# Optimization experiments

Hardware: AMD Instinct MI355X
Metric: run time of the kernel (lower is better)

Reference implementation:

```python
import jax, jax.numpy as jnp
import numpy as np

N_NODES = 2048
N_EDGES = 32768
DIM = 256
HEADS = 4

PARAM_SHAPES = {
    'Wq': (DIM, DIM), 'bq': (DIM,), 'Wk': (DIM, DIM), 'bk': (DIM,),
    'Wv': (DIM, DIM), 'bv': (DIM,), 'Wo': (DIM, DIM), 'bo': (DIM,),
    'gd_W1': (4, 3), 'gd_b1': (3,), 'gd_W2': (3, HEADS), 'gd_b2': (HEADS,),
    'tw_W1': (2 * DIM, DIM), 'tw_b1': (DIM,), 'tw_W2': (DIM, DIM), 'tw_b2': (DIM,),
    'ne_W1': (4 * DIM, 2 * DIM), 'ne_b1': (2 * DIM,), 'ne_W2': (2 * DIM, DIM), 'ne_b2': (DIM,),
    'att_W1': (2 * DIM // HEADS, 2 * DIM // HEADS), 'att_b1': (2 * DIM // HEADS,),
    'att_W2': (DIM // HEADS, 2 * DIM // HEADS), 'att_b2': (DIM // HEADS,),
    'pe_W': (DIM, DIM), 'pe_b': (DIM,), 'pq_W': (DIM, DIM), 'pq_b': (DIM,),
    'pv_W': (DIM, DIM), 'pv_b': (DIM,),
    'pr_W1': (2 * DIM, 2 * DIM), 'pr_b1': (2 * DIM,), 'pr_W2': (2 * DIM, DIM), 'pr_b2': (DIM,),
}


def _lin(x, W, b):
    return x @ W + b


def _mlp2(x, W1, b1, W2, b2):  # Linear-ReLU-Linear (build_mlp, on_last=False)
    return _lin(jnp.maximum(_lin(x, W1, b1), 0.0), W2, b2)


def setup_inputs() -> dict:
    key = jax.random.key(0)
    ks = iter(jax.random.split(key, 64))
    rng = np.random.default_rng(0)
    half = N_EDGES // 2
    s = rng.integers(0, N_NODES, half)
    d = rng.integers(0, N_NODES, half)
    # reciprocal edge pairs so the reverse-edge lookup path is exercised
    edge_index = jnp.asarray(np.stack([np.concatenate([s, d]), np.concatenate([d, s])]), dtype=jnp.int32)
    inp = {
        'node_f': jax.random.normal(next(ks), (N_NODES, DIM), jnp.float32),
        'edge_f': jax.random.normal(next(ks), (N_EDGES, DIM), jnp.float32),
        'coords': jax.random.normal(next(ks), (N_NODES, 3), jnp.float32),
        'edge_index': edge_index,
        'num_heads': HEADS,
    }
    for name, shp in PARAM_SHAPES.items():
        inp[name] = jax.random.normal(next(ks), shp, jnp.float32) * 0.02
    return inp


def _forward(node_f, edge_f, coords, edge_index, num_heads,
             Wq, bq, Wk, bk, Wv, bv, Wo, bo,
             gd_W1, gd_b1, gd_W2, gd_b2,
             tw_W1, tw_b1, tw_W2, tw_b2,
             ne_W1, ne_b1, ne_W2, ne_b2,
             att_W1, att_b1, att_W2, att_b2,
             pe_W, pe_b, pq_W, pq_b, pv_W, pv_b,
             pr_W1, pr_b1, pr_W2, pr_b2):
    N, Dn = node_f.shape
    E, De = edge_f.shape
    H = num_heads
    dh = Wq.shape[1] // H
    src, dst = edge_index[0], edge_index[1]

    # --- NodeUpdate: distance-aware MHSA over all node pairs (batch=1) ---
    q = _lin(node_f, Wq, bq).reshape(N, H, dh)
    k = _lin(node_f, Wk, bk).reshape(N, H, dh)
    v = _lin(node_f, Wv, bv).reshape(N, H, dh)
    diff = coords[:, None, :] - coords[None, :, :]  # [N,N,3]
    sq = jnp.sum(diff * diff, axis=-1, keepdims=True)
    dist = jnp.where(sq > 0, jnp.sqrt(jnp.where(sq > 0, sq, 1.0)), 0.0)
    dmask = _mlp2(jnp.concatenate([diff, dist], -1), gd_W1, gd_b1, gd_W2, gd_b2)  # [N,N,H]
    scores = jnp.einsum('nhd,mhd->hnm', q, k) / float(dh) ** 0.5 + dmask.transpose(2, 0, 1)
    attn = jax.nn.softmax(scores, axis=-1)
    mhsa = _lin(jnp.einsum('hnm,mhd->nhd', attn, v).reshape(N, H * dh), Wo, bo)

    # --- TwinningEdgeAttention: per-node mean of outgoing / incoming edge feats ---
    ones = jnp.ones((E,), edge_f.dtype)
    cnt_s = jnp.maximum(jax.ops.segment_sum(ones, src, num_segments=N), 1.0)
    cnt_d = jnp.maximum(jax.ops.segment_sum(ones, dst, num_segments=N), 1.0)
    sub_mean = jax.ops.segment_sum(edge_f, src, num_segments=N) / cnt_s[:, None]
    obj_mean = jax.ops.segment_sum(edge_f, dst, num_segments=N) / cnt_d[:, None]
    edge_att = jax.nn.sigmoid(_mlp2(jnp.concatenate([sub_mean, obj_mean], -1), tw_W1, tw_b1, tw_W2, tw_b2))
    node_out = jnp.maximum(mhsa, 0.0) * edge_att  # [N, Dn]

    # --- GraphEdgeAttenNetwork ---
    x_i = node_f[src]
    x_j = node_f[dst]
    # reverse-edge matching (vectorized replacement of the python double loop)
    table = jnp.zeros((N * N,), jnp.int32).at[src * N + dst].set(jnp.arange(E, dtype=jnp.int32) + 1)
    rev = table[dst * N + src]
    rev_feat = jnp.where((rev > 0)[:, None], edge_f[jnp.maximum(rev - 1, 0)], 0.0)
    edge_out = _mlp2(jnp.concatenate([x_i, edge_f, rev_feat, x_j], -1), ne_W1, ne_b1, ne_W2, ne_b2)

    value = _lin(x_j, pv_W, pv_b)  # [E, Da]
    query = _lin(x_i, pq_W, pq_b).reshape(E, Dn // H, H)
    edgep = _lin(edge_f, pe_W, pe_b).reshape(E, De // H, H)
    qe = jnp.concatenate([query, edgep], axis=1)  # [E, d_n+d_e, H]
    # conv1d(kernel=1) MLP over channel axis, ReLU between layers
    h = jnp.maximum(jnp.einsum('ech,oc->eoh', qe, att_W1) + att_b1[None, :, None], 0.0)
    prob = jax.nn.softmax(jnp.einsum('ech,oc->eoh', h, att_W2) + att_b2[None, :, None], axis=1)  # [E, d_o, H]
    msg = prob.reshape(E, -1) * value
    agg = jax.ops.segment_max(msg, src, num_segments=N)
    agg = jnp.where(jnp.isfinite(agg), agg, 0.0)  # empty segments -> 0 (torch scatter_max fill)
    xx = _mlp2(jnp.concatenate([node_f, agg], -1), pr_W1, pr_b1, pr_W2, pr_b2)
    return node_out, edge_out, xx


def reference(node_f, edge_f, coords, edge_index, num_heads,
              Wq, bq, Wk, bk, Wv, bv, Wo, bo,
              gd_W1, gd_b1, gd_W2, gd_b2,
              tw_W1, tw_b1, tw_W2, tw_b2,
              ne_W1, ne_b1, ne_W2, ne_b2,
              att_W1, att_b1, att_W2, att_b2,
              pe_W, pe_b, pq_W, pq_b, pv_W, pv_b,
              pr_W1, pr_b1, pr_W2, pr_b2):
    return _forward(node_f, edge_f, coords, edge_index, num_heads,
                    Wq, bq, Wk, bk, Wv, bv, Wo, bo,
                    gd_W1, gd_b1, gd_W2, gd_b2,
                    tw_W1, tw_b1, tw_W2, tw_b2,
                    ne_W1, ne_b1, ne_W2, ne_b2,
                    att_W1, att_b1, att_W2, att_b2,
                    pe_W, pe_b, pq_W, pq_b, pv_W, pv_b,
                    pr_W1, pr_b1, pr_W2, pr_b2)
```

## Files before the change

kernel.cpp:

```cpp
#include <hip/hip_runtime.h>

#define NN 2048
#define NE 32768
#define DIM 256
#define NH 4

typedef unsigned short u16;
typedef __attribute__((ext_vector_type(4))) unsigned short u16x4;
typedef __attribute__((ext_vector_type(8))) short bf16x8;
typedef __attribute__((ext_vector_type(4))) float f32x4;

typedef __attribute__((address_space(1))) const unsigned int g_as1;
typedef __attribute__((address_space(3))) unsigned int l_as3;

__device__ __forceinline__ void gload16(const u16* g, u16* l) {
  __builtin_amdgcn_global_load_lds((g_as1*)g, (l_as3*)l, 16, 0, 0);
}

__device__ __forceinline__ u16 f2bf(float f) {
  unsigned u = __float_as_uint(f);
  unsigned r = u + 0x7FFFu + ((u >> 16) & 1u);
  return (u16)(r >> 16);
}
__device__ __forceinline__ float bf2f(u16 b) {
  return __uint_as_float(((unsigned)b) << 16);
}

struct GB { const u16* A; const int* idx; long ld; long aoffz; };

template<int BNF, int EPI>
__global__ __launch_bounds__(256) void gemm_bf(
    GB ga, const u16* __restrict__ Bt, long bld, long boffz,
    const float* __restrict__ bias, void* __restrict__ Cp, long ldc, long coffz,
    int K, float scale)
{
  __shared__ u16 As[128 * 64];
  __shared__ u16 Bs[32 * BNF * 64];

  const int tid = threadIdx.x;
  const int wid = tid >> 6, lane = tid & 63;
  const int bz = blockIdx.z;
  const int m0 = blockIdx.y * 128;
  const int n0 = blockIdx.x * (32 * BNF);
  const int wr = wid >> 1, wc = wid & 1;
  const int l15 = lane & 15, l4 = lane >> 4;

  const u16* asrc[4];
  #pragma unroll
  for (int c = 0; c < 4; ++c) {
    int rl = c*32 + wid*8 + (lane >> 3);
    int row = ga.idx ? ga.idx[m0 + rl] : (m0 + rl);
    int c16s = (lane & 7) ^ (rl & 7);
    asrc[c] = ga.A + ga.aoffz * bz + (long)row * ga.ld + c16s * 8;
  }
  const u16* bsrc[BNF];
  #pragma unroll
  for (int c = 0; c < BNF; ++c) {
    int rl = c*32 + wid*8 + (lane >> 3);
    int c16s = (lane & 7) ^ (rl & 7);
    bsrc[c] = Bt + boffz * bz + (long)(n0 + rl) * bld + c16s * 8;
  }

  f32x4 acc[4][BNF] = {};

  for (int k0 = 0; k0 < K; k0 += 64) {
    #pragma unroll
    for (int c = 0; c < 4; ++c)
      gload16(asrc[c] + k0, &As[(c*32 + wid*8) * 64]);
    #pragma unroll
    for (int c = 0; c < BNF; ++c)
      gload16(bsrc[c] + k0, &Bs[(c*32 + wid*8) * 64]);
    __syncthreads();

    #pragma unroll
    for (int kk = 0; kk < 2; ++kk) {
      bf16x8 af[4], bfr[BNF];
      #pragma unroll
      for (int i = 0; i < 4; ++i) {
        int r = wr*64 + i*16 + l15;
        af[i] = *(const bf16x8*)&As[r*64 + (((kk*4 + l4) ^ (r & 7)) * 8)];
      }
      #pragma unroll
      for (int j = 0; j < BNF; ++j) {
        int r = wc*(16*BNF) + j*16 + l15;
        bfr[j] = *(const bf16x8*)&Bs[r*64 + (((kk*4 + l4) ^ (r & 7)) * 8)];
      }
      #pragma unroll
      for (int i = 0; i < 4; ++i)
        #pragma unroll
        for (int j = 0; j < BNF; ++j)
          acc[i][j] = __builtin_amdgcn_mfma_f32_16x16x32_bf16(af[i], bfr[j], acc[i][j], 0, 0, 0);
    }
    __syncthreads();
  }

  #pragma unroll
  for (int j = 0; j < BNF; ++j) {
    const int col = n0 + wc*(16*BNF) + j*16 + l15;
    const float bb = bias ? bias[col] : 0.f;
    #pragma unroll
    for (int i = 0; i < 4; ++i) {
      #pragma unroll
      for (int r = 0; r < 4; ++r) {
        const int m = m0 + wr*64 + i*16 + l4*4 + r;
        float v = acc[i][j][r] * scale + bb;
        if constexpr (EPI == 1) v = fmaxf(v, 0.f);
        if constexpr (EPI == 2) v = 1.f / (1.f + expf(-v));
        if constexpr (EPI == 0 || EPI == 2)
          ((float*)Cp)[coffz*bz + (long)m*ldc + col] = v;
        else if constexpr (EPI == 4)
          ((u16*)Cp)[((long)(col & 3) * NE + m) * ldc + (col >> 2) + coffz] = f2bf(v);
        else if constexpr (EPI == 8) {
          if (col < 256)
            ((float*)Cp)[(long)m*256 + (col & 3)*64 + (col >> 2)] = v;
          else {
            u16* qb = (u16*)((float*)Cp + (long)NN*256);
            int c2 = col - 256;
            qb[((long)(c2 & 3)*NN + m)*64 + (c2 >> 2)] = f2bf(v);
          }
        }
        else
          ((u16*)Cp)[coffz*bz + (long)m*ldc + col] = f2bf(v);
      }
    }
  }
}

__global__ __launch_bounds__(256) void flash_k(
    const u16* __restrict__ qkv,
    const u16* __restrict__ vT,
    const float4* __restrict__ pk,
    const float* __restrict__ gW1, const float* __restrict__ gb1,
    const float* __restrict__ gW2, const float* __restrict__ gb2,
    float* __restrict__ Op,
    float2* __restrict__ ml)
{
  __shared__ u16 Qls[64*64];
  __shared__ u16 Kls[128*64];
  __shared__ u16 Vls[2][64*64];
  __shared__ u16 Pls[4][16*128];

  const int tid = threadIdx.x, wid = tid >> 6, lane = tid & 63;
  const int h  = blockIdx.x & 3;
  const int m0 = (blockIdx.x >> 2) * 64;
  const int part = blockIdx.y;
  const int l15 = lane & 15, l4 = lane >> 4;
  const int rl8 = wid*8 + (lane >> 3);
  const int c8  = lane & 7;

  #pragma unroll
  for (int c = 0; c < 2; ++c) {
    int r = c*32 + rl8;
    gload16(qkv + (long)(m0 + r)*768 + h*64 + ((c8 ^ (r & 7))*8), &Qls[(c*32 + wid*8)*64]);
  }
  __syncthreads();
  bf16x8 qf[2];
  {
    int r = wid*16 + l15;
    qf[0] = *(const bf16x8*)&Qls[r*64 + (((0*4 + l4) ^ (r & 7))*8)];
    qf[1] = *(const bf16x8*)&Qls[r*64 + (((1*4 + l4) ^ (r & 7))*8)];
  }

  const float b10 = gb1[0], b11 = gb1[1], b12 = gb1[2];
  const float w30 = gW1[9], w31 = gW1[10], w32 = gW1[11];
  const float w20 = gW2[0*4+h], w21 = gW2[1*4+h], w22 = gW2[2*4+h];
  const float b2h = gb2[h];
  float4 rp0[4], rp1[4];
  #pragma unroll
  for (int r = 0; r < 4; ++r) {
    int qrow = m0 + wid*16 + l4*4 + r;
    rp0[r] = pk[qrow*2]; rp1[r] = pk[qrow*2 + 1];
  }

  float mrun[4] = {-1e30f, -1e30f, -1e30f, -1e30f};
  float lrun[4] = {};
  f32x4 pa[4] = {};

  for (int t = 0; t < 2; ++t) {
    const int n0 = part*256 + t*128;
    #pragma unroll
    for (int c = 0; c < 4; ++c) {
      int r = c*32 + rl8;
      gload16(qkv + (long)(n0 + r)*768 + 256 + h*64 + ((c8 ^ (r & 7))*8),
              &Kls[(c*32 + wid*8)*64]);
    }
    #pragma unroll
    for (int hh = 0; hh < 2; ++hh)
      #pragma unroll
      for (int c = 0; c < 2; ++c) {
        int r = c*32 + rl8;
        gload16(vT + (long)(h*64 + r)*NN + n0 + hh*64 + ((c8 ^ (r & 7))*8),
                &Vls[hh][(c*32 + wid*8)*64]);
      }
    __syncthreads();

    f32x4 sa[8] = {};
    #pragma unroll
    for (int kk = 0; kk < 2; ++kk) {
      #pragma unroll
      for (int j = 0; j < 8; ++j) {
        int r = j*16 + l15;
        bf16x8 bf = *(const bf16x8*)&Kls[r*64 + (((kk*4 + l4) ^ (r & 7))*8)];
        sa[j] = __builtin_amdgcn_mfma_f32_16x16x32_bf16(qf[kk], bf, sa[j], 0, 0, 0);
      }
    }

    float rowmx[4] = {-1e30f, -1e30f, -1e30f, -1e30f};
    #pragma unroll
    for (int j = 0; j < 8; ++j) {
      int n = n0 + j*16 + l15;
      float4 cp0 = pk[n*2], cp1 = pk[n*2 + 1];
      #pragma unroll
      for (int r = 0; r < 4; ++r) {
        float dot = rp0[r].x*cp0.x + rp0[r].y*cp0.y + rp0[r].z*cp0.z;
        float sq = rp0[r].w + cp0.w - 2.f*dot;
        float dist = sq > 0.f ? sq * __frsqrt_rn(sq) : 0.f;
        float h0 = fmaxf(b10 + rp1[r].x - cp1.x + dist*w30, 0.f);
        float h1 = fmaxf(b11 + rp1[r].y - cp1.y + dist*w31, 0.f);
        float h2 = fmaxf(b12 + rp1[r].z - cp1.z + dist*w32, 0.f);
        float s = sa[j][r]*0.125f + b2h + h0*w20 + h1*w21 + h2*w22;
        sa[j][r] = s;
        rowmx[r] = fmaxf(rowmx[r], s);
      }
    }
    #pragma unroll
    for (int w = 1; w < 16; w <<= 1)
      #pragma unroll
      for (int r = 0; r < 4; ++r)
        rowmx[r] = fmaxf(rowmx[r], __shfl_xor(rowmx[r], w));

    float fac[4], rs[4] = {};
    #pragma unroll
    for (int r = 0; r < 4; ++r) {
      float mnew = fmaxf(mrun[r], rowmx[r]);
      fac[r] = __expf(mrun[r] - mnew);
      mrun[r] = mnew;
    }
    #pragma unroll
    for (int j = 0; j < 8; ++j)
      #pragma unroll
      for (int r = 0; r < 4; ++r) {
        float p = __expf(sa[j][r] - mrun[r]);
        sa[j][r] = p;
        rs[r] += p;
      }
    #pragma unroll
    for (int w = 1; w < 16; w <<= 1)
      #pragma unroll
      for (int r = 0; r < 4; ++r)
        rs[r] += __shfl_xor(rs[r], w);
    #pragma unroll
    for (int r = 0; r < 4; ++r) lrun[r] = lrun[r]*fac[r] + rs[r];
    #pragma unroll
    for (int j2 = 0; j2 < 4; ++j2)
      #pragma unroll
      for (int r = 0; r < 4; ++r)
        pa[j2][r] *= fac[r];

    #pragma unroll
    for (int j = 0; j < 8; ++j)
      #pragma unroll
      for (int r = 0; r < 4; ++r) {
        int qr = l4*4 + r, n = j*16 + l15;
        Pls[wid][qr*128 + (((n >> 3) ^ (qr & 7))*8) + (n & 7)] = f2bf(sa[j][r]);
      }
    #pragma unroll
    for (int ks = 0; ks < 4; ++ks) {
      bf16x8 paf = *(const bf16x8*)&Pls[wid][l15*128 + (((ks*4 + l4) ^ (l15 & 7))*8)];
      #pragma unroll
      for (int j2 = 0; j2 < 4; ++j2) {
        int r = j2*16 + l15;
        bf16x8 vf = *(const bf16x8*)&Vls[ks >> 1][r*64 + ((((ks & 1)*4 + l4) ^ (r & 7))*8)];
        pa[j2] = __builtin_amdgcn_mfma_f32_16x16x32_bf16(paf, vf, pa[j2], 0, 0, 0);
      }
    }
    __syncthreads();
  }

  #pragma unroll
  for (int j2 = 0; j2 < 4; ++j2)
    #pragma unroll
    for (int r = 0; r < 4; ++r) {
      int m = m0 + wid*16 + l4*4 + r;
      Op[((long)part*NN + m)*256 + h*64 + j2*16 + l15] = pa[j2][r];
    }
  if (l15 == 0) {
    #pragma unroll
    for (int r = 0; r < 4; ++r) {
      int m = m0 + wid*16 + l4*4 + r;
      ml[((long)part*NN + m)*4 + h] = make_float2(mrun[r], lrun[r]);
    }
  }
}

__global__ __launch_bounds__(256) void comb_k(const float* __restrict__ Op,
    const float2* __restrict__ ml, u16* __restrict__ attn) {
  int n = blockIdx.x, t = threadIdx.x, h = t >> 6;
  float m[8], l[8];
  #pragma unroll
  for (int p = 0; p < 8; ++p) { float2 v = ml[((long)p*NN + n)*4 + h]; m[p] = v.x; l[p] = v.y; }
  float M = m[0];
  #pragma unroll
  for (int p = 1; p < 8; ++p) M = fmaxf(M, m[p]);
  float L = 0.f, o = 0.f;
  #pragma unroll
  for (int p = 0; p < 8; ++p) {
    float w = __expf(m[p] - M);
    L += w * l[p];
    o += w * Op[((long)p*NN + n)*256 + t];
  }
  attn[(long)n*256 + t] = f2bf(o / L);
}

__global__ __launch_bounds__(64) void attedge_k(
    const u16* __restrict__ qN, const u16* __restrict__ ep,
    const float* __restrict__ valNp, const int* __restrict__ ei,
    const u16* __restrict__ W1, const float* __restrict__ b1,
    const u16* __restrict__ W2, const float* __restrict__ b2,
    u16* __restrict__ msgP)
{
  __shared__ u16 As[32*128];
  const int lane = threadIdx.x;
  const int h = blockIdx.y;
  const int e0 = blockIdx.x * 32;
  const int l15 = lane & 15, l4 = lane >> 4;

  #pragma unroll
  for (int p = 0; p < 8; ++p) {
    int R0 = p*4;
    int r  = R0 + (lane >> 4);
    int cd = lane & 15;
    int cs = ((cd & 7) ^ (r & 7)) | (cd & 8);
    const u16* src = (cs < 8)
        ? qN + ((long)h*NN + ei[e0 + r])*64 + cs*8
        : ep + ((long)h*NE + e0 + r)*64 + (cs & 7)*8;
    gload16(src, &As[R0*128]);
  }
  __syncthreads();

  f32x4 acc1[2][8] = {};
  #pragma unroll
  for (int kk = 0; kk < 4; ++kk) {
    bf16x8 af[2], bfr[8];
    #pragma unroll
    for (int i = 0; i < 2; ++i) {
      int rA = i*16 + l15;
      int cg = kk*4 + l4;
      int cd = ((cg & 7) ^ (rA & 7)) | (cg & 8);
      af[i] = *(const bf16x8*)&As[rA*128 + cd*8];
    }
    #pragma unroll
    for (int j = 0; j < 8; ++j)
      bfr[j] = *(const bf16x8*)&W1[(long)(j*16 + l15)*128 + kk*32 + l4*8];
    #pragma unroll
    for (int i = 0; i < 2; ++i)
      #pragma unroll
      for (int j = 0; j < 8; ++j)
        acc1[i][j] = __builtin_amdgcn_mfma_f32_16x16x32_bf16(af[i], bfr[j], acc1[i][j], 0, 0, 0);
  }
  __syncthreads();
  #pragma unroll
  for (int i = 0; i < 2; ++i)
    #pragma unroll
    for (int j = 0; j < 8; ++j) {
      int n = j*16 + l15;
      float bb = b1[n];
      #pragma unroll
      for (int r = 0; r < 4; ++r) {
        int m = i*16 + l4*4 + r;
        int cg = n >> 3;
        int cd = ((cg & 7) ^ (m & 7)) | (cg & 8);
        As[m*128 + cd*8 + (n & 7)] = f2bf(fmaxf(acc1[i][j][r] + bb, 0.f));
      }
    }
  __syncthreads();

  f32x4 acc2[2][4] = {};
  #pragma unroll
  for (int kk = 0; kk < 4; ++kk) {
    bf16x8 af[2], bfr[4];
    #pragma unroll
    for (int i = 0; i < 2; ++i) {
      int rA = i*16 + l15;
      int cg = kk*4 + l4;
      int cd = ((cg & 7) ^ (rA & 7)) | (cg & 8);
      af[i] = *(const bf16x8*)&As[rA*128 + cd*8];
    }
    #pragma unroll
    for (int j = 0; j < 4; ++j)
      bfr[j] = *(const bf16x8*)&W2[(long)(j*16 + l15)*128 + kk*32 + l4*8];
    #pragma unroll
    for (int i = 0; i < 2; ++i)
      #pragma unroll
      for (int j = 0; j < 4; ++j)
        acc2[i][j] = __builtin_amdgcn_mfma_f32_16x16x32_bf16(af[i], bfr[j], acc2[i][j], 0, 0, 0);
  }

  #pragma unroll
  for (int i = 0; i < 2; ++i) {
    float mx[4] = {-1e30f,-1e30f,-1e30f,-1e30f};
    #pragma unroll
    for (int j = 0; j < 4; ++j) {
      float bb = b2[j*16 + l15];
      #pragma unroll
      for (int r = 0; r < 4; ++r) {
        acc2[i][j][r] += bb;
        mx[r] = fmaxf(mx[r], acc2[i][j][r]);
      }
    }
    #pragma unroll
    for (int w = 1; w < 16; w <<= 1)
      #pragma unroll
      for (int r = 0; r < 4; ++r) mx[r] = fmaxf(mx[r], __shfl_xor(mx[r], w));
    float sum[4] = {};
    #pragma unroll
    for (int j = 0; j < 4; ++j)
      #pragma unroll
      for (int r = 0; r < 4; ++r) {
        float p = __expf(acc2[i][j][r] - mx[r]);
        acc2[i][j][r] = p; sum[r] += p;
      }
    #pragma unroll
    for (int w = 1; w < 16; w <<= 1)
      #pragma unroll
      for (int r = 0; r < 4; ++r) sum[r] += __shfl_xor(sum[r], w);
    #pragma unroll
    for (int r = 0; r < 4; ++r) {
      int m = i*16 + l4*4 + r;
      int e = e0 + m;
      int dst = ei[NE + e];
      float inv = 1.f / sum[r];
      #pragma unroll
      for (int j = 0; j < 4; ++j) {
        int o = j*16 + l15;
        float v = valNp[(long)dst*256 + h*64 + o];
        msgP[(long)e*256 + h*64 + o] = f2bf(acc2[i][j][r] * inv * v);
      }
    }
  }
}

__global__ __launch_bounds__(256) void gemm_ne(
    const u16* __restrict__ nbf, const u16* __restrict__ ebf, const u16* __restrict__ zbuf,
    const int* __restrict__ ei, const int* __restrict__ rev,
    const u16* __restrict__ Bt, const float* __restrict__ bias, u16* __restrict__ C)
{
  __shared__ u16 As[2][128 * 64];
  __shared__ u16 Bs[2][128 * 64];
  const int tid = threadIdx.x, wid = tid >> 6, lane = tid & 63;
  const int lin = blockIdx.y * 4 + blockIdx.x;
  const int xcd = lin & 7, seq = lin >> 3;
  const int m0 = (xcd*32 + (seq >> 2)) * 128;
  const int n0 = (seq & 3) * 128;
  const int wr = wid >> 1, wc = wid & 1, l15 = lane & 15, l4 = lane >> 4;

  const u16* asrc[4][4];
  #pragma unroll
  for (int c = 0; c < 4; ++c) {
    int rl = c*32 + wid*8 + (lane >> 3);
    int m = m0 + rl;
    int c16s = ((lane & 7) ^ (rl & 7)) * 8;
    int si = ei[m], di = ei[NE + m], rv = rev[m];
    asrc[0][c] = nbf + (long)si * 256 + c16s;
    asrc[1][c] = ebf + (long)m * 256 + c16s;
    asrc[2][c] = (rv >= 0 ? ebf + (long)rv * 256 : zbuf) + c16s;
    asrc[3][c] = nbf + (long)di * 256 + c16s;
  }
  const u16* bsrc[4];
  #pragma unroll
  for (int c = 0; c < 4; ++c) {
    int rl = c*32 + wid*8 + (lane >> 3);
    int c16s = (lane & 7) ^ (rl & 7);
    bsrc[c] = Bt + (long)(n0 + rl) * 1024 + c16s * 8;
  }

  f32x4 acc[4][4] = {};

#define NE_STAGE(BUF, IT) do {                                                  \
    const int seg_ = (IT) >> 2, kt_ = (IT) & 3;                                 \
    _Pragma("unroll")                                                           \
    for (int c = 0; c < 4; ++c)                                                 \
      gload16(asrc[seg_][c] + kt_*64, &As[BUF][(c*32 + wid*8) * 64]);           \
    _Pragma("unroll")                                                           \
    for (int c = 0; c < 4; ++c)                                                 \
      gload16(bsrc[c] + seg_*256 + kt_*64, &Bs[BUF][(c*32 + wid*8) * 64]);      \
  } while (0)

  NE_STAGE(0, 0);
  #pragma unroll
  for (int it = 0; it < 16; ++it) {
    const int b = it & 1;
    if (it < 15) {
      NE_STAGE(b ^ 1, it + 1);
      asm volatile("s_waitcnt vmcnt(8)" ::: "memory");
    } else {
      asm volatile("s_waitcnt vmcnt(0)" ::: "memory");
    }
    __builtin_amdgcn_s_barrier();
    asm volatile("" ::: "memory");
    #pragma unroll
    for (int kk = 0; kk < 2; ++kk) {
      bf16x8 af[4], bfr[4];
      #pragma unroll
      for (int i = 0; i < 4; ++i) {
        int r = wr*64 + i*16 + l15;
        af[i] = *(const bf16x8*)&As[b][r*64 + (((kk*4 + l4) ^ (r & 7)) * 8)];
      }
      #pragma unroll
      for (int j = 0; j < 4; ++j) {
        int r = wc*64 + j*16 + l15;
        bfr[j] = *(const bf16x8*)&Bs[b][r*64 + (((kk*4 + l4) ^ (r & 7)) * 8)];
      }
      #pragma unroll
      for (int i = 0; i < 4; ++i)
        #pragma unroll
        for (int j = 0; j < 4; ++j)
          acc[i][j] = __builtin_amdgcn_mfma_f32_16x16x32_bf16(af[i], bfr[j], acc[i][j], 0, 0, 0);
    }
    asm volatile("" ::: "memory");
    __builtin_amdgcn_s_barrier();
  }
#undef NE_STAGE

  #pragma unroll
  for (int j = 0; j < 4; ++j) {
    const int col = n0 + wc*64 + j*16 + l15;
    const float bb = bias[col];
    #pragma unroll
    for (int i = 0; i < 4; ++i) {
      #pragma unroll
      for (int r = 0; r < 4; ++r) {
        const int m = m0 + wr*64 + i*16 + l4*4 + r;
        C[(long)m*512 + col] = f2bf(fmaxf(acc[i][j][r] + bb, 0.f));
      }
    }
  }
}

struct PrepEnt { const float* src; void* dst; int K; int N; int ntiles; int op; };
struct PrepDesc { PrepEnt e[24]; int n; };

__global__ __launch_bounds__(256) void wprep_k(PrepDesc d) {
  __shared__ float t[32][33];
  int b = blockIdx.x;
  int ei = 0;
  while (ei < d.n && b >= d.e[ei].ntiles) { b -= d.e[ei].ntiles; ++ei; }
  if (ei >= d.n) return;
  PrepEnt E = d.e[ei];
  int tid = threadIdx.x;
  if (E.op == 0) {
    int kt = E.K >> 5;
    int bk = (b % kt) * 32, bn = (b / kt) * 32;
    int tx = tid & 31, ty = tid >> 5;
    #pragma unroll
    for (int i = ty; i < 32; i += 8) t[i][tx] = E.src[(long)(bk + i) * E.N + bn + tx];
    __syncthreads();
    u16* dst = (u16*)E.dst;
    #pragma unroll
    for (int i = ty; i < 32; i += 8) dst[(long)(bn + i) * E.K + bk + tx] = f2bf(t[tx][i]);
  } else if (E.op == 1) {
    long i = (long)b * 256 + tid;
    long n4 = ((long)E.K * E.N) >> 2;
    if (i < n4) {
      float4 v = ((const float4*)E.src)[i];
      u16x4 o = { f2bf(v.x), f2bf(v.y), f2bf(v.z), f2bf(v.w) };
      ((u16x4*)E.dst)[i] = o;
    }
  } else if (E.op == 3) {
    long i = (long)b * 256 + tid;
    long n4 = ((long)E.K * E.N) >> 2;
    if (i < n4) {
      float4 v = ((const float4*)E.src)[i];
      long row = i >> 6;
      long col = (i & 63) * 4;
      u16x4 o = { f2bf(v.x), f2bf(v.y), f2bf(v.z), f2bf(v.w) };
      *(u16x4*)((u16*)E.dst + row*512 + col) = o;
    }
  } else {
    int i = b * 256 + tid;
    if (i < E.N) ((float*)E.dst)[i] = E.src[i];
  }
}

__global__ void geo_k(const float* __restrict__ C3, const float* __restrict__ gW1,
                      float* __restrict__ geo) {
  int n = blockIdx.x * 256 + threadIdx.x;
  if (n >= NN) return;
  float cx = C3[3*n], cy = C3[3*n+1], cz = C3[3*n+2];
  float s = cx*cx + cy*cy + cz*cz;
  float a0 = cx*gW1[0] + cy*gW1[3] + cz*gW1[6];
  float a1 = cx*gW1[1] + cy*gW1[4] + cz*gW1[7];
  float a2 = cx*gW1[2] + cy*gW1[5] + cz*gW1[8];
  float4* g = (float4*)(geo + (long)n*8);
  g[0] = make_float4(cx, cy, cz, s);
  g[1] = make_float4(a0, a1, a2, 0.f);
}

__global__ __launch_bounds__(256) void transb_k(const u16* __restrict__ src,
                                                u16* __restrict__ dst) {
  __shared__ u16 t[32][34];
  int bm = blockIdx.x * 32, bc = blockIdx.y * 32;
  int tx = threadIdx.x & 31, ty = threadIdx.x >> 5;
  #pragma unroll
  for (int i = ty; i < 32; i += 8) t[i][tx] = src[(long)(bm+i)*768 + 512 + bc + tx];
  __syncthreads();
  #pragma unroll
  for (int i = ty; i < 32; i += 8) dst[(long)(bc+i)*NN + bm + tx] = t[tx][i];
}

__global__ void count_k(const int* __restrict__ ei, int* __restrict__ cs,
                        int* __restrict__ cd) {
  int e = blockIdx.x * 256 + threadIdx.x;
  atomicAdd(&cs[ei[e]], 1);
  atomicAdd(&cd[ei[NE + e]], 1);
}

__global__ __launch_bounds__(256) void scan2_k(const int* __restrict__ cnt_all,
    int* __restrict__ start_all, int* __restrict__ cursor_all) {
  const int* cnt = cnt_all + blockIdx.x * NN;
  int* start  = start_all + blockIdx.x * (NN + 1);
  int* cursor = cursor_all + blockIdx.x * NN;
  __shared__ int part[256];
  int t = threadIdx.x;
  int loc[8]; int s = 0;
  #pragma unroll
  for (int i = 0; i < 8; ++i) { int v = cnt[t*8 + i]; loc[i] = s; s += v; }
  part[t] = s;
  __syncthreads();
  if (t == 0) { int a = 0; for (int i = 0; i < 256; ++i) { int v = part[i]; part[i] = a; a += v; } }
  __syncthreads();
  int base = part[t];
  #pragma unroll
  for (int i = 0; i < 8; ++i) { start[t*8+i] = base + loc[i]; cursor[t*8+i] = base + loc[i]; }
  if (t == 255) start[NN] = base + s;
}

__global__ void scatter2_k(const int* __restrict__ ei, int* __restrict__ cur_s,
    int* __restrict__ cur_d, int* __restrict__ eids_s, int* __restrict__ eids_d) {
  int e = blockIdx.x * 256 + threadIdx.x;
  int p = atomicAdd(&cur_s[ei[e]], 1);
  eids_s[p] = e;
  int q = atomicAdd(&cur_d[ei[NE + e]], 1);
  eids_d[q] = e;
}

__global__ __launch_bounds__(256) void twmean_k(const u16* __restrict__ ebf,
    const int* __restrict__ start_s, const int* __restrict__ eids_s,
    const int* __restrict__ start_d, const int* __restrict__ eids_d,
    u16* __restrict__ twA)
{
  int n = blockIdx.x, t = threadIdx.x;
  int b0 = start_s[n], e0 = start_s[n+1];
  float s = 0.f;
  for (int i = b0; i < e0; ++i)
    s += bf2f(ebf[(long)eids_s[i]*256 + t]);
  twA[(long)n*512 + t] = f2bf(s / fmaxf((float)(e0 - b0), 1.f));
  int b1 = start_d[n], e1 = start_d[n+1];
  float s2 = 0.f;
  for (int i = b1; i < e1; ++i)
    s2 += bf2f(ebf[(long)eids_d[i]*256 + t]);
  twA[(long)n*512 + 256 + t] = f2bf(s2 / fmaxf((float)(e1 - b1), 1.f));
}

__global__ void node_out_k(const float* mh, const float* ea, float* out) {
  long i = (long)blockIdx.x * 256 + threadIdx.x;
  out[i] = fmaxf(mh[i], 0.f) * ea[i];
}

__global__ void scat_k(const int* ei, int* tbl) {
  int e = blockIdx.x * 256 + threadIdx.x;
  atomicMax(&tbl[(long)ei[e] * NN + ei[NE + e]], e + 1);
}

__global__ void rev_k(const int* ei, const int* tbl, int* rev) {
  int e = blockIdx.x * 256 + threadIdx.x;
  rev[e] = tbl[(long)ei[NE + e] * NN + ei[e]] - 1;
}

__global__ __launch_bounds__(256) void agg_k(const int* __restrict__ start,
    const int* __restrict__ eids, const u16* __restrict__ msgP, u16* __restrict__ prA) {
  int n = blockIdx.x, t = threadIdx.x;
  int b = start[n], e_ = start[n+1];
  float mx = -1e30f;
  for (int i = b; i < e_; ++i) {
    int e = eids[i];
    mx = fmaxf(mx, bf2f(msgP[(long)e*256 + t]));
  }
  int c = (t & 63) * 4 + (t >> 6);
  prA[(long)n*512 + 256 + c] = (e_ > b) ? f2bf(mx) : f2bf(0.f);
}

static GB gb(const u16* A, const int* idx, long ld, long aoffz) {
  GB g; g.A = A; g.idx = idx; g.ld = ld; g.aoffz = aoffz; return g;
}

extern "C" void kernel_launch(void* const* d_in, const int* in_sizes, int n_in,
                              void* d_out, int out_size, void* d_ws, size_t ws_size,
                              hipStream_t stream) {
  (void)in_sizes; (void)n_in; (void)out_size; (void)ws_size;

  const float* node_f = (const float*)d_in[0];
  const float* edge_f = (const float*)d_in[1];
  const float* coords = (const float*)d_in[2];
  const int*   ei     = (const int*)d_in[3];
  const float* Wq = (const float*)d_in[5];  const float* bq = (const float*)d_in[6];
  const float* Wk = (const float*)d_in[7];  const float* bk = (const float*)d_in[8];
  const float* Wv = (const float*)d_in[9];  const float* bv = (const float*)d_in[10];
  const float* Wo = (const float*)d_in[11]; const float* bo = (const float*)d_in[12];
  const float* gd_W1 = (const float*)d_in[13]; const float* gd_b1 = (const float*)d_in[14];
  const float* gd_W2 = (const float*)d_in[15]; const float* gd_b2 = (const float*)d_in[16];
  const float* tw_W1 = (const float*)d_in[17]; const float* tw_b1 = (const float*)d_in[18];
  const float* tw_W2 = (const float*)d_in[19]; const float* tw_b2 = (const float*)d_in[20];
  const float* ne_W1 = (const float*)d_in[21]; const float* ne_b1 = (const float*)d_in[22];
  const float* ne_W2 = (const float*)d_in[23]; const float* ne_b2 = (const float*)d_in[24];
  const float* att_W1 = (const float*)d_in[25]; const float* att_b1 = (const float*)d_in[26];
  const float* att_W2 = (const float*)d_in[27]; const float* att_b2 = (const float*)d_in[28];
  const float* pe_W = (const float*)d_in[29]; const float* pe_b = (const float*)d_in[30];
  const float* pq_W = (const float*)d_in[31]; const float* pq_b = (const float*)d_in[32];
  const float* pv_W = (const float*)d_in[33]; const float* pv_b = (const float*)d_in[34];
  const float* pr_W1 = (const float*)d_in[35]; const float* pr_b1 = (const float*)d_in[36];
  const float* pr_W2 = (const float*)d_in[37]; const float* pr_b2 = (const float*)d_in[38];

  char* WB = (char*)d_ws;
  float* out = (float*)d_out;
  float* out_node = out;
  float* out_edge = out + (long)NN*DIM;
  float* out_xx   = out + (long)NN*DIM + (long)NE*DIM;

  const long sz_R1 = 4L*NN*NN*4;
  const long sz_R2 = 4L*NN*NN*2;
  const long sz_R3 = 4L*NE*128*2;
  const long R1 = 0, R2 = R1 + sz_R1, R3 = R2 + sz_R2;

  float*  Opart = (float*)(WB + R1);
  float2* mlbuf = (float2*)(WB + R1 + 8L*NN*256*4);
  u16*    msgP  = (u16*)(WB + R1);
  u16*   nehid  = (u16*)(WB + R2);
  int*   tbl    = (int*)(WB + R3);
  u16*   ep     = (u16*)(WB + R3);
  u16*   edge_bf= (u16*)(WB + R3 + (long)NN*NN*4);

  long cur = R3 + sz_R3;
  auto alloc = [&](long bytes) { long o = cur; cur += (bytes + 255) & ~255L; return o; };

  long o_sub = alloc(2L*NN*DIM*4);
  u16* qkv_bf  = (u16*)(WB + o_sub);
  u16* vT      = qkv_bf + (long)NN*768;
  u16* attn_bf = vT + (long)NN*DIM;

  long o_cs  = alloc(2L*NN*4);
  int* cs_i = (int*)(WB + o_cs); int* cd_i = cs_i + NN;
  long o_mh  = alloc((long)NN*DIM*4);  float* mhsa = (float*)(WB + o_mh);
  long o_ea  = alloc((long)NN*DIM*4);  float* eatt = (float*)(WB + o_ea);
  long o_rv  = alloc((long)NE*4);      int* rev = (int*)(WB + o_rv);
  long o_st  = alloc(2L*(NN+1)*4);     int* start_s = (int*)(WB + o_st);
  int* start_d = start_s + (NN + 1);
  long o_cu  = alloc(2L*NN*4);         int* cursor_s = (int*)(WB + o_cu);
  int* cursor_d = cursor_s + NN;
  long o_eid = alloc(2L*NE*4);         int* eids_s = (int*)(WB + o_eid);
  int* eids_d = eids_s + NE;
  long o_zb  = alloc(1024);            u16* zbuf = (u16*)(WB + o_zb);
  long o_geo = alloc((long)NN*8*4);    float* geo = (float*)(WB + o_geo);
  long o_nbf = alloc((long)NN*DIM*2);  u16* node_bf = (u16*)(WB + o_nbf);
  long o_twA = alloc((long)NN*512*2);  u16* twA = (u16*)(WB + o_twA);
  long o_twh = alloc((long)NN*DIM*2);  u16* twh = (u16*)(WB + o_twh);
  long o_prA = alloc((long)NN*512*2);  u16* prA = (u16*)(WB + o_prA);
  long o_prh = alloc((long)NN*512*2);  u16* prh = (u16*)(WB + o_prh);
  long o_vN  = alloc((long)NN*256*4 + 4L*NN*64*2);
  float* valN = (float*)(WB + o_vN);
  u16*   qN   = (u16*)(valN + (long)NN*256);

  u16* qkv_t = (u16*)(WB + alloc(3L*DIM*DIM*2));
  u16* Wo_t  = (u16*)(WB + alloc(DIM*DIM*2));
  u16* tw1_t = (u16*)(WB + alloc(DIM*512*2));
  u16* tw2_t = (u16*)(WB + alloc(DIM*DIM*2));
  u16* ne1_t = (u16*)(WB + alloc(512L*1024*2));
  u16* ne2_t = (u16*)(WB + alloc(DIM*512*2));
  u16* pe_t  = (u16*)(WB + alloc(DIM*DIM*2));
  u16* pvq_t = (u16*)(WB + alloc(2L*DIM*DIM*2));
  u16* pr1_t = (u16*)(WB + alloc(512L*512*2));
  u16* pr2_t = (u16*)(WB + alloc(DIM*512*2));
  u16* a1_bf = (u16*)(WB + alloc(128*128*2));
  u16* a2_bf = (u16*)(WB + alloc(64*128*2));
  float* qkvb = (float*)(WB + alloc(768*4));
  float* pvqb = (float*)(WB + alloc(512*4));

  hipMemsetAsync(cs_i, 0, 2L*NN*4, stream);
  hipMemsetAsync(tbl, 0, (long)NN*NN*4, stream);
  hipMemsetAsync(zbuf, 0, 1024, stream);

  PrepDesc pd{}; int ne_ = 0; int tot = 0;
  auto addT = [&](const float* s, u16* d, int K, int N) {
    pd.e[ne_] = { s, d, K, N, (K/32)*(N/32), 0 }; tot += pd.e[ne_].ntiles; ++ne_;
  };
  auto addC = [&](const float* s, u16* d, long elems) {
    int nt = (int)((elems/4 + 255) / 256);
    pd.e[ne_] = { s, d, 1, (int)elems, nt, 1 }; tot += nt; ++ne_;
  };
  auto addB = [&](const float* s, float* d, int n) {
    pd.e[ne_] = { s, d, 1, n, (n + 255)/256, 2 }; tot += pd.e[ne_].ntiles; ++ne_;
  };
  addT(Wq, qkv_t,               DIM, DIM);
  addT(Wk, qkv_t + DIM*DIM,     DIM, DIM);
  addT(Wv, qkv_t + 2*DIM*DIM,   DIM, DIM);
  addT(Wo, Wo_t, DIM, DIM);
  addT(tw_W1, tw1_t, 512, DIM);
  addT(tw_W2, tw2_t, DIM, DIM);
  addT(ne_W1, ne1_t, 1024, 512);
  addT(ne_W2, ne2_t, 512, DIM);
  addT(pe_W, pe_t, DIM, DIM);
  addT(pv_W, pvq_t,             DIM, DIM);
  addT(pq_W, pvq_t + DIM*DIM,   DIM, DIM);
  addT(pr_W1, pr1_t, 512, 512);
  addT(pr_W2, pr2_t, 512, DIM);
  addC(att_W1, a1_bf, 128*128);
  addC(att_W2, a2_bf, 64*128);
  addC(node_f, node_bf, (long)NN*DIM);
  addC(edge_f, edge_bf, (long)NE*DIM);
  addB(bq, qkvb, 256); addB(bk, qkvb + 256, 256); addB(bv, qkvb + 512, 256);
  addB(pv_b, pvqb, 256); addB(pq_b, pvqb + 256, 256);
  pd.e[ne_] = { node_f, prA, NN, 256, (int)(((long)NN*256/4 + 255)/256), 3 };
  tot += pd.e[ne_].ntiles; ++ne_;
  pd.n = ne_;
  wprep_k<<<tot, 256, 0, stream>>>(pd);
  geo_k<<<NN/256, 256, 0, stream>>>(coords, gd_W1, geo);

  count_k<<<NE/256, 256, 0, stream>>>(ei, cs_i, cd_i);
  scan2_k<<<2, 256, 0, stream>>>(cs_i, start_s, cursor_s);
  scatter2_k<<<NE/256, 256, 0, stream>>>(ei, cursor_s, cursor_d, eids_s, eids_d);
  twmean_k<<<NN, 256, 0, stream>>>(edge_bf, start_s, eids_s, start_d, eids_d, twA);
  gemm_bf<4,1><<<dim3(2,16,1), 256, 0, stream>>>(gb(twA, nullptr, 512, 0), tw1_t, 512, 0,
      tw_b1, twh, DIM, 0, 512, 1.f);
  gemm_bf<4,2><<<dim3(2,16,1), 256, 0, stream>>>(gb(twh, nullptr, DIM, 0), tw2_t, DIM, 0,
      tw_b2, eatt, DIM, 0, DIM, 1.f);

  gemm_bf<4,5><<<dim3(6,16,1), 256, 0, stream>>>(gb(node_bf, nullptr, DIM, 0), qkv_t, DIM, 0,
      qkvb, qkv_bf, 768, 0, DIM, 1.f);
  transb_k<<<dim3(64,8), 256, 0, stream>>>(qkv_bf, vT);
  flash_k<<<dim3(128,8), 256, 0, stream>>>(qkv_bf, vT, (const float4*)geo,
      gd_W1, gd_b1, gd_W2, gd_b2, Opart, mlbuf);
  comb_k<<<NN, 256, 0, stream>>>(Opart, mlbuf, attn_bf);
  gemm_bf<4,0><<<dim3(2,16,1), 256, 0, stream>>>(gb(attn_bf, nullptr, DIM, 0), Wo_t, DIM, 0,
      bo, mhsa, DIM, 0, DIM, 1.f);
  node_out_k<<<NN, 256, 0, stream>>>(mhsa, eatt, out_node);

  scat_k<<<NE/256, 256, 0, stream>>>(ei, tbl);
  rev_k<<<NE/256, 256, 0, stream>>>(ei, tbl, rev);
  gemm_ne<<<dim3(4,256,1), 256, 0, stream>>>(node_bf, edge_bf, zbuf, ei, rev,
      ne1_t, ne_b1, nehid);
  gemm_bf<4,0><<<dim3(2,256,1), 256, 0, stream>>>(gb(nehid, nullptr, 512, 0), ne2_t, 512, 0,
      ne_b2, out_edge, DIM, 0, 512, 1.f);

  gemm_bf<4,8><<<dim3(4,16,1), 256, 0, stream>>>(gb(node_bf, nullptr, DIM, 0), pvq_t, DIM, 0,
      pvqb, valN, 256, 0, DIM, 1.f);
  gemm_bf<4,4><<<dim3(2,256,1), 256, 0, stream>>>(gb(edge_bf, nullptr, DIM, 0), pe_t, DIM, 0,
      pe_b, ep, 64, 0, DIM, 1.f);
  attedge_k<<<dim3(NE/32, NH), 64, 0, stream>>>(qN, ep, valN, ei,
      a1_bf, att_b1, a2_bf, att_b2, msgP);
  agg_k<<<NN, 256, 0, stream>>>(start_s, eids_s, msgP, prA);

  gemm_bf<4,1><<<dim3(4,16,1), 256, 0, stream>>>(gb(prA, nullptr, 512, 0), pr1_t, 512, 0,
      pr_b1, prh, 512, 0, 512, 1.f);
  gemm_bf<4,0><<<dim3(2,16,1), 256, 0, stream>>>(gb(prh, nullptr, 512, 0), pr2_t, 512, 0,
      pr_b2, out_xx, DIM, 0, 512, 1.f);
}
```

Measured before the change: 398.4 us.

## Widen edge GEMM to 8 waves, load Q directly, split tw-mean roles

The edge-MLP first-layer GEMM now runs 512 threads per block as a 2x4 wave grid, so each wave holds half as many accumulators and issues half as many tile loads; the wait counts are adjusted to match. The flash kernel drops its LDS staging of Q and reads the query fragments straight from global memory, which removes a barrier and frees shared memory. The two-way neighbour mean kernel now launches one block per node and per role instead of doing both sums in sequence, doubling parallelism. The workspace allocation is resized to the exact buffer sizes it needs.

```diff
diff --git a/kernel.cpp b/kernel.cpp
--- a/kernel.cpp
+++ b/kernel.cpp
@@ -135,7 +135,6 @@
     float* __restrict__ Op,
     float2* __restrict__ ml)
 {
-  __shared__ u16 Qls[64*64];
   __shared__ u16 Kls[128*64];
   __shared__ u16 Vls[2][64*64];
   __shared__ u16 Pls[4][16*128];
@@ -148,17 +147,11 @@
   const int rl8 = wid*8 + (lane >> 3);
   const int c8  = lane & 7;
 
-  #pragma unroll
-  for (int c = 0; c < 2; ++c) {
-    int r = c*32 + rl8;
-    gload16(qkv + (long)(m0 + r)*768 + h*64 + ((c8 ^ (r & 7))*8), &Qls[(c*32 + wid*8)*64]);
-  }
-  __syncthreads();
   bf16x8 qf[2];
   {
-    int r = wid*16 + l15;
-    qf[0] = *(const bf16x8*)&Qls[r*64 + (((0*4 + l4) ^ (r & 7))*8)];
-    qf[1] = *(const bf16x8*)&Qls[r*64 + (((1*4 + l4) ^ (r & 7))*8)];
+    const u16* qp = qkv + (long)(m0 + wid*16 + l15)*768 + h*64 + l4*8;
+    qf[0] = *(const bf16x8*)(qp);
+    qf[1] = *(const bf16x8*)(qp + 32);
   }
 
   const float b10 = gb1[0], b11 = gb1[1], b12 = gb1[2];
@@ -440,7 +433,7 @@
   }
 }
 
-__global__ __launch_bounds__(256) void gemm_ne(
+__global__ __launch_bounds__(512) void gemm_ne(
     const u16* __restrict__ nbf, const u16* __restrict__ ebf, const u16* __restrict__ zbuf,
     const int* __restrict__ ei, const int* __restrict__ rev,
     const u16* __restrict__ Bt, const float* __restrict__ bias, u16* __restrict__ C)
@@ -452,12 +445,12 @@
   const int xcd = lin & 7, seq = lin >> 3;
   const int m0 = (xcd*32 + (seq >> 2)) * 128;
   const int n0 = (seq & 3) * 128;
-  const int wr = wid >> 1, wc = wid & 1, l15 = lane & 15, l4 = lane >> 4;
-
-  const u16* asrc[4][4];
-  #pragma unroll
-  for (int c = 0; c < 4; ++c) {
-    int rl = c*32 + wid*8 + (lane >> 3);
+  const int wr = wid >> 2, wc = wid & 3, l15 = lane & 15, l4 = lane >> 4;
+
+  const u16* asrc[4][2];
+  #pragma unroll
+  for (int c = 0; c < 2; ++c) {
+    int rl = c*64 + wid*8 + (lane >> 3);
     int m = m0 + rl;
     int c16s = ((lane & 7) ^ (rl & 7)) * 8;
     int si = ei[m], di = ei[NE + m], rv = rev[m];
@@ -466,24 +459,24 @@
     asrc[2][c] = (rv >= 0 ? ebf + (long)rv * 256 : zbuf) + c16s;
     asrc[3][c] = nbf + (long)di * 256 + c16s;
   }
-  const u16* bsrc[4];
-  #pragma unroll
-  for (int c = 0; c < 4; ++c) {
-    int rl = c*32 + wid*8 + (lane >> 3);
+  const u16* bsrc[2];
+  #pragma unroll
+  for (int c = 0; c < 2; ++c) {
+    int rl = c*64 + wid*8 + (lane >> 3);
     int c16s = (lane & 7) ^ (rl & 7);
     bsrc[c] = Bt + (long)(n0 + rl) * 1024 + c16s * 8;
   }
 
-  f32x4 acc[4][4] = {};
+  f32x4 acc[4][2] = {};
 
 #define NE_STAGE(BUF, IT) do {                                                  \
     const int seg_ = (IT) >> 2, kt_ = (IT) & 3;                                 \
     _Pragma("unroll")                                                           \
-    for (int c = 0; c < 4; ++c)                                                 \
-      gload16(asrc[seg_][c] + kt_*64, &As[BUF][(c*32 + wid*8) * 64]);           \
+    for (int c = 0; c < 2; ++c)                                                 \
+      gload16(asrc[seg_][c] + kt_*64, &As[BUF][(c*64 + wid*8) * 64]);           \
     _Pragma("unroll")                                                           \
-    for (int c = 0; c < 4; ++c)                                                 \
-      gload16(bsrc[c] + seg_*256 + kt_*64, &Bs[BUF][(c*32 + wid*8) * 64]);      \
+    for (int c = 0; c < 2; ++c)                                                 \
+      gload16(bsrc[c] + seg_*256 + kt_*64, &Bs[BUF][(c*64 + wid*8) * 64]);      \
   } while (0)
 
   NE_STAGE(0, 0);
@@ -492,7 +485,7 @@
     const int b = it & 1;
     if (it < 15) {
       NE_STAGE(b ^ 1, it + 1);
-      asm volatile("s_waitcnt vmcnt(8)" ::: "memory");
+      asm volatile("s_waitcnt vmcnt(4)" ::: "memory");
     } else {
       asm volatile("s_waitcnt vmcnt(0)" ::: "memory");
     }
@@ -500,21 +493,21 @@
     asm volatile("" ::: "memory");
     #pragma unroll
     for (int kk = 0; kk < 2; ++kk) {
-      bf16x8 af[4], bfr[4];
+      bf16x8 af[4], bfr[2];
       #pragma unroll
       for (int i = 0; i < 4; ++i) {
         int r = wr*64 + i*16 + l15;
         af[i] = *(const bf16x8*)&As[b][r*64 + (((kk*4 + l4) ^ (r & 7)) * 8)];
       }
       #pragma unroll
-      for (int j = 0; j < 4; ++j) {
-        int r = wc*64 + j*16 + l15;
+      for (int j = 0; j < 2; ++j) {
+        int r = wc*32 + j*16 + l15;
         bfr[j] = *(const bf16x8*)&Bs[b][r*64 + (((kk*4 + l4) ^ (r & 7)) * 8)];
       }
       #pragma unroll
       for (int i = 0; i < 4; ++i)
         #pragma unroll
-        for (int j = 0; j < 4; ++j)
+        for (int j = 0; j < 2; ++j)
           acc[i][j] = __builtin_amdgcn_mfma_f32_16x16x32_bf16(af[i], bfr[j], acc[i][j], 0, 0, 0);
     }
     asm volatile("" ::: "memory");
@@ -523,8 +516,8 @@
 #undef NE_STAGE
 
   #pragma unroll
-  for (int j = 0; j < 4; ++j) {
-    const int col = n0 + wc*64 + j*16 + l15;
+  for (int j = 0; j < 2; ++j) {
+    const int col = n0 + wc*32 + j*16 + l15;
     const float bb = bias[col];
     #pragma unroll
     for (int i = 0; i < 4; ++i) {
@@ -649,17 +642,14 @@
     const int* __restrict__ start_d, const int* __restrict__ eids_d,
     u16* __restrict__ twA)
 {
-  int n = blockIdx.x, t = threadIdx.x;
-  int b0 = start_s[n], e0 = start_s[n+1];
+  int n = blockIdx.x, t = threadIdx.x, role = blockIdx.y;
+  const int* start = role ? start_d : start_s;
+  const int* eids  = role ? eids_d  : eids_s;
+  int b0 = start[n], e0 = start[n+1];
   float s = 0.f;
   for (int i = b0; i < e0; ++i)
-    s += bf2f(ebf[(long)eids_s[i]*256 + t]);
-  twA[(long)n*512 + t] = f2bf(s / fmaxf((float)(e0 - b0), 1.f));
-  int b1 = start_d[n], e1 = start_d[n+1];
-  float s2 = 0.f;
-  for (int i = b1; i < e1; ++i)
-    s2 += bf2f(ebf[(long)eids_d[i]*256 + t]);
-  twA[(long)n*512 + 256 + t] = f2bf(s2 / fmaxf((float)(e1 - b1), 1.f));
+    s += bf2f(ebf[(long)eids[i]*256 + t]);
+  twA[(long)n*512 + role*256 + t] = f2bf(s / fmaxf((float)(e0 - b0), 1.f));
 }
 
 __global__ void node_out_k(const float* mh, const float* ea, float* out) {
@@ -743,7 +733,7 @@
   long cur = R3 + sz_R3;
   auto alloc = [&](long bytes) { long o = cur; cur += (bytes + 255) & ~255L; return o; };
 
-  long o_sub = alloc(2L*NN*DIM*4);
+  long o_sub = alloc((long)NN*768*2 + (long)NN*DIM*2 + (long)NN*DIM*2);
   u16* qkv_bf  = (u16*)(WB + o_sub);
   u16* vT      = qkv_bf + (long)NN*768;
   u16* attn_bf = vT + (long)NN*DIM;
@@ -828,7 +818,7 @@
   count_k<<<NE/256, 256, 0, stream>>>(ei, cs_i, cd_i);
   scan2_k<<<2, 256, 0, stream>>>(cs_i, start_s, cursor_s);
   scatter2_k<<<NE/256, 256, 0, stream>>>(ei, cursor_s, cursor_d, eids_s, eids_d);
-  twmean_k<<<NN, 256, 0, stream>>>(edge_bf, start_s, eids_s, start_d, eids_d, twA);
+  twmean_k<<<dim3(NN,2), 256, 0, stream>>>(edge_bf, start_s, eids_s, start_d, eids_d, twA);
   gemm_bf<4,1><<<dim3(2,16,1), 256, 0, stream>>>(gb(twA, nullptr, 512, 0), tw1_t, 512, 0,
       tw_b1, twh, DIM, 0, 512, 1.f);
   gemm_bf<4,2><<<dim3(2,16,1), 256, 0, stream>>>(gb(twh, nullptr, DIM, 0), tw2_t, DIM, 0,
@@ -846,7 +836,7 @@
 
   scat_k<<<NE/256, 256, 0, stream>>>(ei, tbl);
   rev_k<<<NE/256, 256, 0, stream>>>(ei, tbl, rev);
-  gemm_ne<<<dim3(4,256,1), 256, 0, stream>>>(node_bf, edge_bf, zbuf, ei, rev,
+  gemm_ne<<<dim3(4,256,1), 512, 0, stream>>>(node_bf, edge_bf, zbuf, ei, rev,
       ne1_t, ne_b1, nehid);
   gemm_bf<4,0><<<dim3(2,256,1), 256, 0, stream>>>(gb(nehid, nullptr, 512, 0), ne2_t, 512, 0,
       ne_b2, out_edge, DIM, 0, 512, 1.f);
```

New measurement: 385.4 us. 1.03x faster.
